# Kernel tuning notes

Hardware: AMD Instinct MI355X
Metric: run time of the kernel (lower is better)

The kernel has to match this reference:

```python
import jax, jax.numpy as jnp
import numpy as np

N = 50000
E = 800000
IN_C, HID_C, OUT_C = 128, 128, 64


def _glorot(key, shape, gain=1.0):
    fan_in, fan_out = shape[0], shape[1]
    lim = gain * np.sqrt(6.0 / (fan_in + fan_out))
    return jax.random.uniform(key, shape, jnp.float32, -lim, lim)


def setup_inputs() -> dict:
    key = jax.random.key(0)
    ks = jax.random.split(key, 16)
    relu_gain = float(np.sqrt(2.0))
    x = jax.random.normal(ks[0], (N, IN_C), jnp.float32)
    src = jax.random.randint(ks[1], (E,), 0, N, jnp.int64)
    dst = jax.random.randint(ks[2], (E,), 0, N, jnp.int64)
    # layer 0: NGNN_GCNConv(IN_C -> HID_C -> HID_C)
    W0 = _glorot(ks[3], (IN_C, HID_C))
    b0 = jnp.zeros((HID_C,), jnp.float32)
    fcW = _glorot(ks[4], (HID_C, HID_C), relu_gain)
    fcb = jax.random.uniform(ks[5], (HID_C,), jnp.float32, -1, 1) / np.sqrt(HID_C)
    fc2W = _glorot(ks[6], (HID_C, HID_C), relu_gain)
    fc2b = jax.random.uniform(ks[7], (HID_C,), jnp.float32, -1, 1) / np.sqrt(HID_C)
    # layer 1: GraphConv(HID_C -> HID_C)
    W1 = _glorot(ks[8], (HID_C, HID_C))
    b1 = jnp.zeros((HID_C,), jnp.float32)
    # layer 2: GraphConv(HID_C -> OUT_C)
    W2 = _glorot(ks[9], (HID_C, OUT_C))
    b2 = jnp.zeros((OUT_C,), jnp.float32)
    return dict(x=x, src=src, dst=dst, W0=W0, b0=b0, fcW=fcW, fcb=fcb,
                fc2W=fc2W, fc2b=fc2b, W1=W1, b1=b1, W2=W2, b2=b2)


def _degree_norms(src, dst):
    ones = jnp.ones((E,), jnp.float32)
    deg_out = jnp.clip(jax.ops.segment_sum(ones, src, num_segments=N), 1.0)
    deg_in = jnp.clip(jax.ops.segment_sum(ones, dst, num_segments=N), 1.0)
    return jax.lax.rsqrt(deg_out), jax.lax.rsqrt(deg_in)


def _graph_conv(x, W, b, src, dst, nsrc, ndst):
    # DGL GraphConv, norm='both': out = D_in^{-1/2} A (D_out^{-1/2} x W) + b
    h = (x * nsrc[:, None]) @ W            # [N, out_c]
    agg = jax.ops.segment_sum(h[src], dst, num_segments=N)  # gather + scatter-add
    return agg * ndst[:, None] + b


def reference(x, src, dst, W0, b0, fcW, fcb, fc2W, fc2b, W1, b1, W2, b2):
    nsrc, ndst = _degree_norms(src, dst)
    # layer 0: NGNN_GCNConv -> relu (dropout: eval-mode identity)
    h = _graph_conv(x, W0, b0, src, dst, nsrc, ndst)
    h = jax.nn.relu(h)
    h = jax.nn.relu(h @ fcW + fcb)
    h = h @ fc2W + fc2b
    h = jax.nn.relu(h)
    # layer 1: GraphConv -> relu
    h = jax.nn.relu(_graph_conv(h, W1, b1, src, dst, nsrc, ndst))
    # layer 2: GraphConv (no activation)
    return _graph_conv(h, W2, b2, src, dst, nsrc, ndst)
```

## Files before the change

kernel.cpp:

```cpp
#include <hip/hip_runtime.h>
#include <hip/hip_bf16.h>

#define NN 50000
#define NE 800000
#define PAD 56

typedef __attribute__((ext_vector_type(8))) short bf16x8;
typedef __attribute__((ext_vector_type(4))) float f32x4;
typedef __attribute__((ext_vector_type(8))) unsigned short u16x8;

__device__ __forceinline__ unsigned short f2bf(float f) {
    __hip_bfloat16 h = __float2bfloat16(f);
    return *(unsigned short*)&h;
}
__device__ __forceinline__ float bf2f(unsigned short u) {
    unsigned int w = ((unsigned int)u) << 16;
    return __uint_as_float(w);
}

__device__ __forceinline__ void split8(const float* __restrict__ p, bf16x8& h8, bf16x8& l8) {
    float4 v0 = *(const float4*)p;
    float4 v1 = *(const float4*)(p + 4);
    float f[8] = {v0.x, v0.y, v0.z, v0.w, v1.x, v1.y, v1.z, v1.w};
#pragma unroll
    for (int i = 0; i < 8; ++i) {
        unsigned short h = f2bf(f[i]);
        h8[i] = (short)h;
        l8[i] = (short)f2bf(f[i] - bf2f(h));
    }
}

#define SRC_BLK 64
#define SRC_CHUNK 12500
#define DST_BLK 160
#define DST_CHUNK 5000
#define DEG_WORDS 12500
#define GEMM0_BLK 782
#define CVW_ELEMS 57344
#define CVW_BLK 224

__global__ __launch_bounds__(256) void hists_kernel(
    const int* __restrict__ src, const int* __restrict__ dst,
    unsigned* __restrict__ psrc, unsigned* __restrict__ pdst,
    const float* __restrict__ x, const float* __restrict__ W0, unsigned short* __restrict__ Hb,
    const float* __restrict__ fcW, const float* __restrict__ fc2W,
    const float* __restrict__ W1, const float* __restrict__ W2,
    unsigned short* __restrict__ wp_hi, unsigned short* __restrict__ wp_lo) {
    __shared__ unsigned hist[DEG_WORDS];
    const int bid = blockIdx.x;
    const int tid = threadIdx.x;
    if (bid < SRC_BLK + DST_BLK) {
        const bool isSrc = bid < SRC_BLK;
        const int dblk = isSrc ? bid : bid - SRC_BLK;
        const int chunk = isSrc ? SRC_CHUNK : DST_CHUNK;
        const int* ep = isSrc ? (src + dblk * SRC_CHUNK) : (dst + dblk * DST_CHUNK);
        unsigned* outp = (isSrc ? psrc : pdst) + (size_t)dblk * DEG_WORDS;
        for (int i = tid; i < DEG_WORDS; i += 256) hist[i] = 0;
        __syncthreads();
        const int4* sp = (const int4*)ep;
        for (int i = tid; i < chunk / 4; i += 256) {
            int4 s = sp[i];
            atomicAdd(&hist[s.x >> 2], 1u << ((s.x & 3) * 8));
            atomicAdd(&hist[s.y >> 2], 1u << ((s.y & 3) * 8));
            atomicAdd(&hist[s.z >> 2], 1u << ((s.z & 3) * 8));
            atomicAdd(&hist[s.w >> 2], 1u << ((s.w & 3) * 8));
        }
        __syncthreads();
        for (int i = tid; i < DEG_WORDS; i += 256) outp[i] = hist[i];
    } else if (bid < SRC_BLK + DST_BLK + CVW_BLK) {
        int t = (bid - SRC_BLK - DST_BLK) * 256 + tid;
        if (t < CVW_ELEMS) {
            int mi = (t < 16384) ? 0 : (t < 32768) ? 1 : (t < 49152) ? 2 : 3;
            int beg = mi * 16384;
            int Cm = (mi == 3) ? 64 : 128;
            int loc = t - beg;
            int k = loc / Cm, c = loc % Cm;
            float v;
            switch (mi) {
                case 0: v = fcW[loc]; break;
                case 1: v = fc2W[loc]; break;
                case 2: v = W1[loc]; break;
                default: v = W2[loc]; break;
            }
            unsigned short h = f2bf(v);
            unsigned short l = f2bf(v - bf2f(h));
            int off = (((c >> 4) * 4 + (k >> 5)) * 64 + ((k & 31) >> 3) * 16 + (c & 15)) * 8 + (k & 7);
            wp_hi[beg + off] = h;
            wp_lo[beg + off] = l;
        }
    } else {
        const int gb = bid - SRC_BLK - DST_BLK - CVW_BLK;
        const int wave = tid >> 6;
        const int lane = tid & 63;
        const int m = lane & 15, kg = lane >> 4;
        const int r0 = gb * 64 + wave * 16;
        int ar = r0 + m;
        ar = (ar < NN) ? ar : (NN - 1);

        bf16x8 ah[4], al[4];
#pragma unroll
        for (int ks = 0; ks < 4; ++ks)
            split8(&x[(size_t)ar * 128 + ks * 32 + kg * 8], ah[ks], al[ks]);

#pragma unroll
        for (int ct = 0; ct < 8; ++ct) {
            f32x4 acc = {0.f, 0.f, 0.f, 0.f};
            const int n = ct * 16 + m;
#pragma unroll
            for (int ks = 0; ks < 4; ++ks) {
                float w[8];
#pragma unroll
                for (int i = 0; i < 8; ++i)
                    w[i] = W0[(size_t)(ks * 32 + kg * 8 + i) * 128 + n];
                bf16x8 bh, bl;
#pragma unroll
                for (int i = 0; i < 8; ++i) {
                    unsigned short h = f2bf(w[i]);
                    bh[i] = (short)h;
                    bl[i] = (short)f2bf(w[i] - bf2f(h));
                }
                acc = __builtin_amdgcn_mfma_f32_16x16x32_bf16(ah[ks], bh, acc, 0, 0, 0);
                acc = __builtin_amdgcn_mfma_f32_16x16x32_bf16(al[ks], bh, acc, 0, 0, 0);
                acc = __builtin_amdgcn_mfma_f32_16x16x32_bf16(ah[ks], bl, acc, 0, 0, 0);
            }
#pragma unroll
            for (int j = 0; j < 4; ++j) {
                const int ra = r0 + 4 * kg + j;
                if (ra < NN) Hb[(size_t)ra * 128 + n] = f2bf(acc[j]);
            }
        }
    }
}

__global__ __launch_bounds__(256) void merge_scan(unsigned* __restrict__ psrc,
                                                  unsigned* __restrict__ pdst,
                                                  int* __restrict__ degout,
                                                  int* __restrict__ cnt) {
    const int idx = blockIdx.x * 256 + threadIdx.x;
    if (idx >= DEG_WORDS) return;
    {
        int a0 = 0, a1 = 0, a2 = 0, a3 = 0;
#pragma unroll 8
        for (int p = 0; p < SRC_BLK; ++p) {
            unsigned w = psrc[(size_t)p * DEG_WORDS + idx];
            a0 += w & 0xFF; a1 += (w >> 8) & 0xFF; a2 += (w >> 16) & 0xFF; a3 += (w >> 24);
        }
        ((int4*)degout)[idx] = make_int4(a0, a1, a2, a3);
    }
    {
        int r0 = 0, r1 = 0, r2 = 0, r3 = 0;
#pragma unroll 8
        for (int p = 0; p < DST_BLK; ++p) {
            const size_t o = (size_t)p * DEG_WORDS + idx;
            unsigned w = pdst[o];
            pdst[o] = (unsigned)r0 | ((unsigned)r1 << 8) | ((unsigned)r2 << 16) | ((unsigned)r3 << 24);
            r0 += w & 0xFF; r1 += (w >> 8) & 0xFF; r2 += (w >> 16) & 0xFF; r3 += (w >> 24);
        }
        ((int4*)cnt)[idx] = make_int4(r0, r1, r2, r3);
    }
}

__global__ __launch_bounds__(256) void fillc_kernel(const int* __restrict__ src,
                                                    const int* __restrict__ dst,
                                                    const unsigned* __restrict__ pdst,
                                                    unsigned short* __restrict__ col) {
    __shared__ unsigned hist[DEG_WORDS];
    const int dblk = blockIdx.x;
    const int tid = threadIdx.x;
    const unsigned* bp = pdst + (size_t)dblk * DEG_WORDS;
    for (int i = tid; i < DEG_WORDS; i += 256) hist[i] = bp[i];
    __syncthreads();
    const int4* sp = (const int4*)(src + dblk * DST_CHUNK);
    const int4* dp = (const int4*)(dst + dblk * DST_CHUNK);
    for (int i = tid; i < DST_CHUNK / 4; i += 256) {
        int4 s = sp[i];
        int4 d = dp[i];
#pragma unroll
        for (int u = 0; u < 4; ++u) {
            const int dd = (u == 0) ? d.x : (u == 1) ? d.y : (u == 2) ? d.z : d.w;
            const int ss = (u == 0) ? s.x : (u == 1) ? s.y : (u == 2) ? s.z : s.w;
            const unsigned sh = (dd & 3) * 8;
            const unsigned old = atomicAdd(&hist[dd >> 2], 1u << sh);
            const int slot = (old >> sh) & 0xFF;
            col[dd * PAD + slot] = (unsigned short)ss;
        }
    }
}

__device__ __forceinline__ void t_write4(float (*T)[128], int lr, int c, float4 v) {
    *(float4*)&T[lr][(((c >> 2) ^ (lr & 31)) << 2)] = v;
}
__device__ __forceinline__ void t_write(float (*T)[128], int lr, int n, float v) {
    T[lr][((((n >> 2) ^ (lr & 31)) << 2) | (n & 3))] = v;
}
__device__ __forceinline__ void split8_lds(const float (*T)[128], int lr, int c, bf16x8& h8, bf16x8& l8) {
    const int c4 = c >> 2, xr = lr & 31;
    float4 v0 = *(const float4*)&T[lr][(c4 ^ xr) << 2];
    float4 v1 = *(const float4*)&T[lr][((c4 + 1) ^ xr) << 2];
    float f[8] = {v0.x, v0.y, v0.z, v0.w, v1.x, v1.y, v1.z, v1.w};
#pragma unroll
    for (int i = 0; i < 8; ++i) {
        unsigned short h = f2bf(f[i]);
        h8[i] = (short)h;
        l8[i] = (short)f2bf(f[i] - bf2f(h));
    }
}

template <int SCALE_SRC>
__device__ __forceinline__ void gather32_to_T(
    float (*T)[128], const unsigned short* __restrict__ H,
    const int* __restrict__ cnt, const int* __restrict__ degout,
    const unsigned short* __restrict__ colp, const float* __restrict__ bias,
    int r0, int N, int tid) {
    const int nl = tid >> 3;
    const int q  = tid & 7;
    int node = r0 + nl;
    node = (node < N) ? node : (N - 1);
    const int deg = cnt[node];
    const unsigned short* cl = colp + node * PAD;
    f32x4 acc[4];
#pragma unroll
    for (int v = 0; v < 4; ++v) acc[v] = (f32x4){0.f, 0.f, 0.f, 0.f};
    const int nch = (deg + 3) >> 2;
    for (int ch = 0; ch < nch; ++ch) {
        const int jb = ch * 4;
        ushort4 si = *(const ushort4*)&cl[jb];
        u16x8 h0[4], h1[4];
        float mm[4];
#pragma unroll
        for (int i = 0; i < 4; ++i) {
            const bool live = (jb + i < deg);
            const unsigned short sv = (i == 0) ? si.x : (i == 1) ? si.y : (i == 2) ? si.z : si.w;
            int s = live ? (int)sv : 0;
            const unsigned short* hp = &H[(size_t)s * 128 + q * 16];
            h0[i] = *(const u16x8*)hp;
            h1[i] = *(const u16x8*)(hp + 8);
            if (SCALE_SRC) {
                int dg = degout[s];
                float r = rsqrtf((float)(dg > 1 ? dg : 1));
                mm[i] = live ? r : 0.f;
            } else {
                mm[i] = live ? 1.f : 0.f;
            }
        }
#pragma unroll
        for (int i = 0; i < 4; ++i) {
#pragma unroll
            for (int k = 0; k < 8; ++k) {
                acc[k >> 2][k & 3] = fmaf(bf2f((unsigned short)h0[i][k]), mm[i], acc[k >> 2][k & 3]);
                acc[2 + (k >> 2)][k & 3] = fmaf(bf2f((unsigned short)h1[i][k]), mm[i], acc[2 + (k >> 2)][k & 3]);
            }
        }
    }
    const float scv = rsqrtf((float)(deg > 1 ? deg : 1));
#pragma unroll
    for (int v = 0; v < 4; ++v) {
        const int c = q * 16 + v * 4;
        const float4 b = *(const float4*)&bias[c];
        float4 o;
        o.x = fmaxf(acc[v][0] * scv + b.x, 0.f);
        o.y = fmaxf(acc[v][1] * scv + b.y, 0.f);
        o.z = fmaxf(acc[v][2] * scv + b.z, 0.f);
        o.w = fmaxf(acc[v][3] * scv + b.w, 0.f);
        t_write4(T, nl, c, o);
    }
}

#define TILE(WH, WL) \
    f32x4 acc = {0.f, 0.f, 0.f, 0.f}; \
    _Pragma("unroll") \
    for (int ks = 0; ks < 4; ++ks) { \
        const size_t base = ((size_t)(CT * 4 + ks) * 64 + lane) * 8; \
        bf16x8 bh = *(const bf16x8*)&WH[base]; \
        bf16x8 bl = *(const bf16x8*)&WL[base]; \
        acc = __builtin_amdgcn_mfma_f32_16x16x32_bf16(ah[ks], bh, acc, 0, 0, 0); \
        acc = __builtin_amdgcn_mfma_f32_16x16x32_bf16(al[ks], bh, acc, 0, 0, 0); \
        acc = __builtin_amdgcn_mfma_f32_16x16x32_bf16(ah[ks], bl, acc, 0, 0, 0); \
    }

#define LOAD_FRAGS_T() \
    _Pragma("unroll") \
    for (int ks = 0; ks < 4; ++ks) \
        split8_lds(T, wr + m, ks * 32 + kg * 8, ah[ks], al[ks]);

__global__ __launch_bounds__(256) void g0f3_kernel(
    const unsigned short* __restrict__ H,
    const int* __restrict__ cnt, const int* __restrict__ degout,
    const unsigned short* __restrict__ colp, const float* __restrict__ b0,
    const unsigned short* __restrict__ fwh, const unsigned short* __restrict__ fwl,
    const float* __restrict__ fcb,
    const unsigned short* __restrict__ f2h, const unsigned short* __restrict__ f2l,
    const float* __restrict__ fc2b,
    const unsigned short* __restrict__ w1h, const unsigned short* __restrict__ w1l,
    unsigned short* __restrict__ Yb, int N) {
    __shared__ float T[32][128];
    const int tid = threadIdx.x;
    const int wave = tid >> 6;
    const int lane = tid & 63;
    const int m = lane & 15, kg = lane >> 4;
    const int rowg = wave >> 1;
    const int colh = wave & 1;
    const int r0 = blockIdx.x * 32;
    const int wr = rowg * 16;

    gather32_to_T<1>(T, H, cnt, degout, colp, b0, r0, N, tid);
    __syncthreads();

    bf16x8 ah[4], al[4];
    LOAD_FRAGS_T();
    __syncthreads();

#pragma unroll
    for (int ct = 0; ct < 4; ++ct) {
        const int CT = colh * 4 + ct;
        TILE(fwh, fwl)
        const int n = CT * 16 + m;
        const float bb = fcb[n];
#pragma unroll
        for (int j = 0; j < 4; ++j)
            t_write(T, wr + 4 * kg + j, n, fmaxf(acc[j] + bb, 0.f));
    }
    __syncthreads();
    LOAD_FRAGS_T();
    __syncthreads();

#pragma unroll
    for (int ct = 0; ct < 4; ++ct) {
        const int CT = colh * 4 + ct;
        TILE(f2h, f2l)
        const int n = CT * 16 + m;
        const float bb = fc2b[n];
#pragma unroll
        for (int j = 0; j < 4; ++j)
            t_write(T, wr + 4 * kg + j, n, fmaxf(acc[j] + bb, 0.f));
    }
    __syncthreads();
    LOAD_FRAGS_T();

#pragma unroll
    for (int ct = 0; ct < 4; ++ct) {
        const int CT = colh * 4 + ct;
        TILE(w1h, w1l)
        const int n = CT * 16 + m;
#pragma unroll
        for (int j = 0; j < 4; ++j) {
            const int ra = r0 + wr + 4 * kg + j;
            if (ra < N) {
                int dg = degout[ra];
                Yb[(size_t)ra * 128 + n] = f2bf(acc[j] * rsqrtf((float)(dg > 1 ? dg : 1)));
            }
        }
    }
}

__global__ __launch_bounds__(256) void g1g2_kernel(
    const unsigned short* __restrict__ H,
    const int* __restrict__ cnt, const int* __restrict__ degout,
    const unsigned short* __restrict__ colp, const float* __restrict__ b1,
    const unsigned short* __restrict__ w2h, const unsigned short* __restrict__ w2l,
    unsigned short* __restrict__ Yb, int N) {
    __shared__ float T[32][128];
    const int tid = threadIdx.x;
    const int wave = tid >> 6;
    const int lane = tid & 63;
    const int m = lane & 15, kg = lane >> 4;
    const int rowg = wave >> 1;
    const int colh = wave & 1;
    const int r0 = blockIdx.x * 32;
    const int wr = rowg * 16;

    gather32_to_T<0>(T, H, cnt, degout, colp, b1, r0, N, tid);
    __syncthreads();

    bf16x8 ah[4], al[4];
    LOAD_FRAGS_T();

#pragma unroll
    for (int ct = 0; ct < 2; ++ct) {
        const int CT = colh * 2 + ct;
        TILE(w2h, w2l)
        const int n = CT * 16 + m;
#pragma unroll
        for (int j = 0; j < 4; ++j) {
            const int ra = r0 + wr + 4 * kg + j;
            if (ra < N) {
                int dg = degout[ra];
                Yb[(size_t)ra * 64 + n] = f2bf(acc[j] * rsqrtf((float)(dg > 1 ? dg : 1)));
            }
        }
    }
}

__global__ __launch_bounds__(256) void gather2_kernel(
    const unsigned short* __restrict__ H, const int* __restrict__ cnt,
    const unsigned short* __restrict__ col,
    const float* __restrict__ bias, float* __restrict__ OUT, int N) {
    constexpr int C = 64, LPN = 8, NPB = 32;
    const int node = blockIdx.x * NPB + threadIdx.x / LPN;
    const int q = threadIdx.x % LPN;
    if (node >= N) return;
    const int deg = cnt[node];
    const unsigned short* cl = col + node * PAD;
    float acc[8];
#pragma unroll
    for (int k = 0; k < 8; ++k) acc[k] = 0.f;
    const int nch = (deg + 7) >> 3;
    for (int ch = 0; ch < nch; ++ch) {
        const int jb = ch * 8;
        u16x8 si = *(const u16x8*)&cl[jb];
        u16x8 hv[8];
        float mm[8];
#pragma unroll
        for (int i = 0; i < 8; ++i) {
            const bool live = (jb + i < deg);
            int s = live ? (int)si[i] : 0;
            hv[i] = *(const u16x8*)&H[(size_t)s * C + q * 8];
            mm[i] = live ? 1.f : 0.f;
        }
#pragma unroll
        for (int i = 0; i < 8; ++i) {
#pragma unroll
            for (int k = 0; k < 8; ++k)
                acc[k] = fmaf(bf2f((unsigned short)hv[i][k]), mm[i], acc[k]);
        }
    }
    const float scv = rsqrtf((float)(deg > 1 ? deg : 1));
    const int cb = q * 8;
    float4 o0, o1;
    const float4 b0 = *(const float4*)&bias[cb];
    const float4 b1 = *(const float4*)&bias[cb + 4];
    o0.x = acc[0] * scv + b0.x; o0.y = acc[1] * scv + b0.y;
    o0.z = acc[2] * scv + b0.z; o0.w = acc[3] * scv + b0.w;
    o1.x = acc[4] * scv + b1.x; o1.y = acc[5] * scv + b1.y;
    o1.z = acc[6] * scv + b1.z; o1.w = acc[7] * scv + b1.w;
    *(float4*)&OUT[(size_t)node * C + cb] = o0;
    *(float4*)&OUT[(size_t)node * C + cb + 4] = o1;
}

extern "C" void kernel_launch(void* const* d_in, const int* in_sizes, int n_in,
                              void* d_out, int out_size, void* d_ws, size_t ws_size,
                              hipStream_t stream) {
    const float* x    = (const float*)d_in[0];
    const int*   src  = (const int*)d_in[1];
    const int*   dst  = (const int*)d_in[2];
    const float* W0   = (const float*)d_in[3];
    const float* b0   = (const float*)d_in[4];
    const float* fcW  = (const float*)d_in[5];
    const float* fcb  = (const float*)d_in[6];
    const float* fc2W = (const float*)d_in[7];
    const float* fc2b = (const float*)d_in[8];
    const float* W1   = (const float*)d_in[9];
    const float* b1   = (const float*)d_in[10];
    const float* W2   = (const float*)d_in[11];
    const float* b2   = (const float*)d_in[12];
    float* out = (float*)d_out;

    char* ws = (char*)d_ws;
    int* cnt    = (int*)ws;
    int* degout = cnt + NN;
    unsigned short* col = (unsigned short*)(degout + NN);
    unsigned short* wp_hi = col + (size_t)NN * PAD;
    unsigned short* wp_lo = wp_hi + CVW_ELEMS;
    size_t p = ((size_t)(2 * NN) * 4 + (size_t)NN * PAD * 2 + (size_t)CVW_ELEMS * 4 + 255) & ~(size_t)255;
    unsigned* psrc = (unsigned*)(ws + p);
    unsigned* pdst = psrc + (size_t)SRC_BLK * DEG_WORDS;
    size_t p1 = (p + (size_t)(SRC_BLK + DST_BLK) * DEG_WORDS * 4 + 255) & ~(size_t)255;
    unsigned short* Hb  = (unsigned short*)(ws + p1);
    unsigned short* Hb2 = Hb + (size_t)NN * 128;

    const unsigned short *fwh = wp_hi,          *fwl = wp_lo;
    const unsigned short *f2h = wp_hi + 16384,  *f2l = wp_lo + 16384;
    const unsigned short *w1h = wp_hi + 32768,  *w1l = wp_lo + 32768;
    const unsigned short *w2h = wp_hi + 49152,  *w2l = wp_lo + 49152;

    hists_kernel<<<SRC_BLK + DST_BLK + CVW_BLK + GEMM0_BLK, 256, 0, stream>>>(
        src, dst, psrc, pdst, x, W0, Hb, fcW, fc2W, W1, W2, wp_hi, wp_lo);
    merge_scan<<<(DEG_WORDS + 255) / 256, 256, 0, stream>>>(psrc, pdst, degout, cnt);
    fillc_kernel<<<DST_BLK, 256, 0, stream>>>(src, dst, pdst, col);

    const int g32 = (NN + 31) / 32;

    g0f3_kernel<<<g32, 256, 0, stream>>>(Hb, cnt, degout, col, b0,
                                         fwh, fwl, fcb, f2h, f2l, fc2b, w1h, w1l, Hb2, NN);
    g1g2_kernel<<<g32, 256, 0, stream>>>(Hb2, cnt, degout, col, b1, w2h, w2l, Hb, NN);
    gather2_kernel<<<g32, 256, 0, stream>>>(Hb, cnt, col, b2, out, NN);
}
```

Measured before the change: 161.2 us.

## Halve rows per block in fused gather+MLP kernels, 16 lanes per node

```diff
diff --git a/kernel.cpp b/kernel.cpp
--- a/kernel.cpp
+++ b/kernel.cpp
@@ -207,34 +207,30 @@
 }
 
 template <int SCALE_SRC>
-__device__ __forceinline__ void gather32_to_T(
+__device__ __forceinline__ void gather16_to_T(
     float (*T)[128], const unsigned short* __restrict__ H,
     const int* __restrict__ cnt, const int* __restrict__ degout,
     const unsigned short* __restrict__ colp, const float* __restrict__ bias,
     int r0, int N, int tid) {
-    const int nl = tid >> 3;
-    const int q  = tid & 7;
+    const int nl = tid >> 4;
+    const int q  = tid & 15;
     int node = r0 + nl;
     node = (node < N) ? node : (N - 1);
     const int deg = cnt[node];
     const unsigned short* cl = colp + node * PAD;
-    f32x4 acc[4];
-#pragma unroll
-    for (int v = 0; v < 4; ++v) acc[v] = (f32x4){0.f, 0.f, 0.f, 0.f};
-    const int nch = (deg + 3) >> 2;
+    f32x4 acc0 = {0.f, 0.f, 0.f, 0.f};
+    f32x4 acc1 = {0.f, 0.f, 0.f, 0.f};
+    const int nch = (deg + 7) >> 3;
     for (int ch = 0; ch < nch; ++ch) {
-        const int jb = ch * 4;
-        ushort4 si = *(const ushort4*)&cl[jb];
-        u16x8 h0[4], h1[4];
-        float mm[4];
-#pragma unroll
-        for (int i = 0; i < 4; ++i) {
+        const int jb = ch * 8;
+        u16x8 si = *(const u16x8*)&cl[jb];
+        u16x8 hv[8];
+        float mm[8];
+#pragma unroll
+        for (int i = 0; i < 8; ++i) {
             const bool live = (jb + i < deg);
-            const unsigned short sv = (i == 0) ? si.x : (i == 1) ? si.y : (i == 2) ? si.z : si.w;
-            int s = live ? (int)sv : 0;
-            const unsigned short* hp = &H[(size_t)s * 128 + q * 16];
-            h0[i] = *(const u16x8*)hp;
-            h1[i] = *(const u16x8*)(hp + 8);
+            int s = live ? (int)si[i] : 0;
+            hv[i] = *(const u16x8*)&H[(size_t)s * 128 + q * 8];
             if (SCALE_SRC) {
                 int dg = degout[s];
                 float r = rsqrtf((float)(dg > 1 ? dg : 1));
@@ -244,26 +240,29 @@
             }
         }
 #pragma unroll
-        for (int i = 0; i < 4; ++i) {
-#pragma unroll
-            for (int k = 0; k < 8; ++k) {
-                acc[k >> 2][k & 3] = fmaf(bf2f((unsigned short)h0[i][k]), mm[i], acc[k >> 2][k & 3]);
-                acc[2 + (k >> 2)][k & 3] = fmaf(bf2f((unsigned short)h1[i][k]), mm[i], acc[2 + (k >> 2)][k & 3]);
+        for (int i = 0; i < 8; ++i) {
+#pragma unroll
+            for (int k = 0; k < 4; ++k) {
+                acc0[k] = fmaf(bf2f((unsigned short)hv[i][k]), mm[i], acc0[k]);
+                acc1[k] = fmaf(bf2f((unsigned short)hv[i][4 + k]), mm[i], acc1[k]);
             }
         }
     }
     const float scv = rsqrtf((float)(deg > 1 ? deg : 1));
-#pragma unroll
-    for (int v = 0; v < 4; ++v) {
-        const int c = q * 16 + v * 4;
-        const float4 b = *(const float4*)&bias[c];
-        float4 o;
-        o.x = fmaxf(acc[v][0] * scv + b.x, 0.f);
-        o.y = fmaxf(acc[v][1] * scv + b.y, 0.f);
-        o.z = fmaxf(acc[v][2] * scv + b.z, 0.f);
-        o.w = fmaxf(acc[v][3] * scv + b.w, 0.f);
-        t_write4(T, nl, c, o);
-    }
+    const int c = q * 8;
+    const float4 b0 = *(const float4*)&bias[c];
+    const float4 b1 = *(const float4*)&bias[c + 4];
+    float4 o0, o1;
+    o0.x = fmaxf(acc0[0] * scv + b0.x, 0.f);
+    o0.y = fmaxf(acc0[1] * scv + b0.y, 0.f);
+    o0.z = fmaxf(acc0[2] * scv + b0.z, 0.f);
+    o0.w = fmaxf(acc0[3] * scv + b0.w, 0.f);
+    o1.x = fmaxf(acc1[0] * scv + b1.x, 0.f);
+    o1.y = fmaxf(acc1[1] * scv + b1.y, 0.f);
+    o1.z = fmaxf(acc1[2] * scv + b1.z, 0.f);
+    o1.w = fmaxf(acc1[3] * scv + b1.w, 0.f);
+    t_write4(T, nl, c, o0);
+    t_write4(T, nl, c + 4, o1);
 }
 
 #define TILE(WH, WL) \
@@ -281,7 +280,7 @@
 #define LOAD_FRAGS_T() \
     _Pragma("unroll") \
     for (int ks = 0; ks < 4; ++ks) \
-        split8_lds(T, wr + m, ks * 32 + kg * 8, ah[ks], al[ks]);
+        split8_lds(T, m, ks * 32 + kg * 8, ah[ks], al[ks]);
 
 __global__ __launch_bounds__(256) void g0f3_kernel(
     const unsigned short* __restrict__ H,
@@ -293,17 +292,14 @@
     const float* __restrict__ fc2b,
     const unsigned short* __restrict__ w1h, const unsigned short* __restrict__ w1l,
     unsigned short* __restrict__ Yb, int N) {
-    __shared__ float T[32][128];
+    __shared__ float T[16][128];
     const int tid = threadIdx.x;
     const int wave = tid >> 6;
     const int lane = tid & 63;
     const int m = lane & 15, kg = lane >> 4;
-    const int rowg = wave >> 1;
-    const int colh = wave & 1;
-    const int r0 = blockIdx.x * 32;
-    const int wr = rowg * 16;
-
-    gather32_to_T<1>(T, H, cnt, degout, colp, b0, r0, N, tid);
+    const int r0 = blockIdx.x * 16;
+
+    gather16_to_T<1>(T, H, cnt, degout, colp, b0, r0, N, tid);
     __syncthreads();
 
     bf16x8 ah[4], al[4];
@@ -311,40 +307,40 @@
     __syncthreads();
 
 #pragma unroll
-    for (int ct = 0; ct < 4; ++ct) {
-        const int CT = colh * 4 + ct;
+    for (int ct = 0; ct < 2; ++ct) {
+        const int CT = wave * 2 + ct;
         TILE(fwh, fwl)
         const int n = CT * 16 + m;
         const float bb = fcb[n];
 #pragma unroll
         for (int j = 0; j < 4; ++j)
-            t_write(T, wr + 4 * kg + j, n, fmaxf(acc[j] + bb, 0.f));
+            t_write(T, 4 * kg + j, n, fmaxf(acc[j] + bb, 0.f));
     }
     __syncthreads();
     LOAD_FRAGS_T();
     __syncthreads();
 
 #pragma unroll
-    for (int ct = 0; ct < 4; ++ct) {
-        const int CT = colh * 4 + ct;
+    for (int ct = 0; ct < 2; ++ct) {
+        const int CT = wave * 2 + ct;
         TILE(f2h, f2l)
         const int n = CT * 16 + m;
         const float bb = fc2b[n];
 #pragma unroll
         for (int j = 0; j < 4; ++j)
-            t_write(T, wr + 4 * kg + j, n, fmaxf(acc[j] + bb, 0.f));
+            t_write(T, 4 * kg + j, n, fmaxf(acc[j] + bb, 0.f));
     }
     __syncthreads();
     LOAD_FRAGS_T();
 
 #pragma unroll
-    for (int ct = 0; ct < 4; ++ct) {
-        const int CT = colh * 4 + ct;
+    for (int ct = 0; ct < 2; ++ct) {
+        const int CT = wave * 2 + ct;
         TILE(w1h, w1l)
         const int n = CT * 16 + m;
 #pragma unroll
         for (int j = 0; j < 4; ++j) {
-            const int ra = r0 + wr + 4 * kg + j;
+            const int ra = r0 + 4 * kg + j;
             if (ra < N) {
                 int dg = degout[ra];
                 Yb[(size_t)ra * 128 + n] = f2bf(acc[j] * rsqrtf((float)(dg > 1 ? dg : 1)));
@@ -359,30 +355,26 @@
     const unsigned short* __restrict__ colp, const float* __restrict__ b1,
     const unsigned short* __restrict__ w2h, const unsigned short* __restrict__ w2l,
     unsigned short* __restrict__ Yb, int N) {
-    __shared__ float T[32][128];
+    __shared__ float T[16][128];
     const int tid = threadIdx.x;
     const int wave = tid >> 6;
     const int lane = tid & 63;
     const int m = lane & 15, kg = lane >> 4;
-    const int rowg = wave >> 1;
-    const int colh = wave & 1;
-    const int r0 = blockIdx.x * 32;
-    const int wr = rowg * 16;
-
-    gather32_to_T<0>(T, H, cnt, degout, colp, b1, r0, N, tid);
+    const int r0 = blockIdx.x * 16;
+
+    gather16_to_T<0>(T, H, cnt, degout, colp, b1, r0, N, tid);
     __syncthreads();
 
     bf16x8 ah[4], al[4];
     LOAD_FRAGS_T();
 
-#pragma unroll
-    for (int ct = 0; ct < 2; ++ct) {
-        const int CT = colh * 2 + ct;
+    {
+        const int CT = wave;
         TILE(w2h, w2l)
         const int n = CT * 16 + m;
 #pragma unroll
         for (int j = 0; j < 4; ++j) {
-            const int ra = r0 + wr + 4 * kg + j;
+            const int ra = r0 + 4 * kg + j;
             if (ra < N) {
                 int dg = degout[ra];
                 Yb[(size_t)ra * 64 + n] = f2bf(acc[j] * rsqrtf((float)(dg > 1 ? dg : 1)));
@@ -478,10 +470,11 @@
     merge_scan<<<(DEG_WORDS + 255) / 256, 256, 0, stream>>>(psrc, pdst, degout, cnt);
     fillc_kernel<<<DST_BLK, 256, 0, stream>>>(src, dst, pdst, col);
 
+    const int g16 = (NN + 15) / 16;
     const int g32 = (NN + 31) / 32;
 
-    g0f3_kernel<<<g32, 256, 0, stream>>>(Hb, cnt, degout, col, b0,
+    g0f3_kernel<<<g16, 256, 0, stream>>>(Hb, cnt, degout, col, b0,
                                          fwh, fwl, fcb, f2h, f2l, fc2b, w1h, w1l, Hb2, NN);
-    g1g2_kernel<<<g32, 256, 0, stream>>>(Hb2, cnt, degout, col, b1, w2h, w2l, Hb, NN);
+    g1g2_kernel<<<g16, 256, 0, stream>>>(Hb2, cnt, degout, col, b1, w2h, w2l, Hb, NN);
     gather2_kernel<<<g32, 256, 0, stream>>>(Hb, cnt, col, b2, out, NN);
 }
```

Measured after the change: 152.5 us. 1.06x faster.

## Give each wave both row tiles in dense layers and even out src histogram split

Applied to the files above, without the earlier changes.

```diff
diff --git a/kernel.cpp b/kernel.cpp
--- a/kernel.cpp
+++ b/kernel.cpp
@@ -30,10 +30,8 @@
     }
 }
 
-#define SRC_BLK 64
-#define SRC_CHUNK 12500
-#define DST_BLK 160
-#define DST_CHUNK 5000
+#define HIST_BLK 160
+#define HIST_CHUNK 5000
 #define DEG_WORDS 12500
 #define GEMM0_BLK 782
 #define CVW_ELEMS 57344
@@ -49,16 +47,15 @@
     __shared__ unsigned hist[DEG_WORDS];
     const int bid = blockIdx.x;
     const int tid = threadIdx.x;
-    if (bid < SRC_BLK + DST_BLK) {
-        const bool isSrc = bid < SRC_BLK;
-        const int dblk = isSrc ? bid : bid - SRC_BLK;
-        const int chunk = isSrc ? SRC_CHUNK : DST_CHUNK;
-        const int* ep = isSrc ? (src + dblk * SRC_CHUNK) : (dst + dblk * DST_CHUNK);
+    if (bid < 2 * HIST_BLK) {
+        const bool isSrc = bid < HIST_BLK;
+        const int dblk = isSrc ? bid : bid - HIST_BLK;
+        const int* ep = (isSrc ? src : dst) + dblk * HIST_CHUNK;
         unsigned* outp = (isSrc ? psrc : pdst) + (size_t)dblk * DEG_WORDS;
         for (int i = tid; i < DEG_WORDS; i += 256) hist[i] = 0;
         __syncthreads();
         const int4* sp = (const int4*)ep;
-        for (int i = tid; i < chunk / 4; i += 256) {
+        for (int i = tid; i < HIST_CHUNK / 4; i += 256) {
             int4 s = sp[i];
             atomicAdd(&hist[s.x >> 2], 1u << ((s.x & 3) * 8));
             atomicAdd(&hist[s.y >> 2], 1u << ((s.y & 3) * 8));
@@ -67,8 +64,8 @@
         }
         __syncthreads();
         for (int i = tid; i < DEG_WORDS; i += 256) outp[i] = hist[i];
-    } else if (bid < SRC_BLK + DST_BLK + CVW_BLK) {
-        int t = (bid - SRC_BLK - DST_BLK) * 256 + tid;
+    } else if (bid < 2 * HIST_BLK + CVW_BLK) {
+        int t = (bid - 2 * HIST_BLK) * 256 + tid;
         if (t < CVW_ELEMS) {
             int mi = (t < 16384) ? 0 : (t < 32768) ? 1 : (t < 49152) ? 2 : 3;
             int beg = mi * 16384;
@@ -89,7 +86,7 @@
             wp_lo[beg + off] = l;
         }
     } else {
-        const int gb = bid - SRC_BLK - DST_BLK - CVW_BLK;
+        const int gb = bid - 2 * HIST_BLK - CVW_BLK;
         const int wave = tid >> 6;
         const int lane = tid & 63;
         const int m = lane & 15, kg = lane >> 4;
@@ -141,7 +138,7 @@
     {
         int a0 = 0, a1 = 0, a2 = 0, a3 = 0;
 #pragma unroll 8
-        for (int p = 0; p < SRC_BLK; ++p) {
+        for (int p = 0; p < HIST_BLK; ++p) {
             unsigned w = psrc[(size_t)p * DEG_WORDS + idx];
             a0 += w & 0xFF; a1 += (w >> 8) & 0xFF; a2 += (w >> 16) & 0xFF; a3 += (w >> 24);
         }
@@ -150,7 +147,7 @@
     {
         int r0 = 0, r1 = 0, r2 = 0, r3 = 0;
 #pragma unroll 8
-        for (int p = 0; p < DST_BLK; ++p) {
+        for (int p = 0; p < HIST_BLK; ++p) {
             const size_t o = (size_t)p * DEG_WORDS + idx;
             unsigned w = pdst[o];
             pdst[o] = (unsigned)r0 | ((unsigned)r1 << 8) | ((unsigned)r2 << 16) | ((unsigned)r3 << 24);
@@ -170,9 +167,9 @@
     const unsigned* bp = pdst + (size_t)dblk * DEG_WORDS;
     for (int i = tid; i < DEG_WORDS; i += 256) hist[i] = bp[i];
     __syncthreads();
-    const int4* sp = (const int4*)(src + dblk * DST_CHUNK);
-    const int4* dp = (const int4*)(dst + dblk * DST_CHUNK);
-    for (int i = tid; i < DST_CHUNK / 4; i += 256) {
+    const int4* sp = (const int4*)(src + dblk * HIST_CHUNK);
+    const int4* dp = (const int4*)(dst + dblk * HIST_CHUNK);
+    for (int i = tid; i < HIST_CHUNK / 4; i += 256) {
         int4 s = sp[i];
         int4 d = dp[i];
 #pragma unroll
@@ -266,22 +263,28 @@
     }
 }
 
-#define TILE(WH, WL) \
-    f32x4 acc = {0.f, 0.f, 0.f, 0.f}; \
+#define TILE2(WH, WL) \
+    f32x4 acc0 = {0.f, 0.f, 0.f, 0.f}; \
+    f32x4 acc1 = {0.f, 0.f, 0.f, 0.f}; \
     _Pragma("unroll") \
     for (int ks = 0; ks < 4; ++ks) { \
         const size_t base = ((size_t)(CT * 4 + ks) * 64 + lane) * 8; \
         bf16x8 bh = *(const bf16x8*)&WH[base]; \
         bf16x8 bl = *(const bf16x8*)&WL[base]; \
-        acc = __builtin_amdgcn_mfma_f32_16x16x32_bf16(ah[ks], bh, acc, 0, 0, 0); \
-        acc = __builtin_amdgcn_mfma_f32_16x16x32_bf16(al[ks], bh, acc, 0, 0, 0); \
-        acc = __builtin_amdgcn_mfma_f32_16x16x32_bf16(ah[ks], bl, acc, 0, 0, 0); \
-    }
-
-#define LOAD_FRAGS_T() \
+        acc0 = __builtin_amdgcn_mfma_f32_16x16x32_bf16(ah0[ks], bh, acc0, 0, 0, 0); \
+        acc1 = __builtin_amdgcn_mfma_f32_16x16x32_bf16(ah1[ks], bh, acc1, 0, 0, 0); \
+        acc0 = __builtin_amdgcn_mfma_f32_16x16x32_bf16(al0[ks], bh, acc0, 0, 0, 0); \
+        acc1 = __builtin_amdgcn_mfma_f32_16x16x32_bf16(al1[ks], bh, acc1, 0, 0, 0); \
+        acc0 = __builtin_amdgcn_mfma_f32_16x16x32_bf16(ah0[ks], bl, acc0, 0, 0, 0); \
+        acc1 = __builtin_amdgcn_mfma_f32_16x16x32_bf16(ah1[ks], bl, acc1, 0, 0, 0); \
+    }
+
+#define LOAD_FRAGS2() \
     _Pragma("unroll") \
-    for (int ks = 0; ks < 4; ++ks) \
-        split8_lds(T, wr + m, ks * 32 + kg * 8, ah[ks], al[ks]);
+    for (int ks = 0; ks < 4; ++ks) { \
+        split8_lds(T, m,      ks * 32 + kg * 8, ah0[ks], al0[ks]); \
+        split8_lds(T, 16 + m, ks * 32 + kg * 8, ah1[ks], al1[ks]); \
+    }
 
 __global__ __launch_bounds__(256) void g0f3_kernel(
     const unsigned short* __restrict__ H,
@@ -298,56 +301,62 @@
     const int wave = tid >> 6;
     const int lane = tid & 63;
     const int m = lane & 15, kg = lane >> 4;
-    const int rowg = wave >> 1;
-    const int colh = wave & 1;
     const int r0 = blockIdx.x * 32;
-    const int wr = rowg * 16;
 
     gather32_to_T<1>(T, H, cnt, degout, colp, b0, r0, N, tid);
     __syncthreads();
 
-    bf16x8 ah[4], al[4];
-    LOAD_FRAGS_T();
-    __syncthreads();
-
-#pragma unroll
-    for (int ct = 0; ct < 4; ++ct) {
-        const int CT = colh * 4 + ct;
-        TILE(fwh, fwl)
+    bf16x8 ah0[4], al0[4], ah1[4], al1[4];
+    LOAD_FRAGS2();
+    __syncthreads();
+
+#pragma unroll
+    for (int ct = 0; ct < 2; ++ct) {
+        const int CT = wave * 2 + ct;
+        TILE2(fwh, fwl)
         const int n = CT * 16 + m;
         const float bb = fcb[n];
 #pragma unroll
-        for (int j = 0; j < 4; ++j)
-            t_write(T, wr + 4 * kg + j, n, fmaxf(acc[j] + bb, 0.f));
-    }
-    __syncthreads();
-    LOAD_FRAGS_T();
-    __syncthreads();
-
-#pragma unroll
-    for (int ct = 0; ct < 4; ++ct) {
-        const int CT = colh * 4 + ct;
-        TILE(f2h, f2l)
+        for (int j = 0; j < 4; ++j) {
+            t_write(T, 4 * kg + j,      n, fmaxf(acc0[j] + bb, 0.f));
+            t_write(T, 16 + 4 * kg + j, n, fmaxf(acc1[j] + bb, 0.f));
+        }
+    }
+    __syncthreads();
+    LOAD_FRAGS2();
+    __syncthreads();
+
+#pragma unroll
+    for (int ct = 0; ct < 2; ++ct) {
+        const int CT = wave * 2 + ct;
+        TILE2(f2h, f2l)
         const int n = CT * 16 + m;
         const float bb = fc2b[n];
 #pragma unroll
-        for (int j = 0; j < 4; ++j)
-            t_write(T, wr + 4 * kg + j, n, fmaxf(acc[j] + bb, 0.f));
-    }
-    __syncthreads();
-    LOAD_FRAGS_T();
-
-#pragma unroll
-    for (int ct = 0; ct < 4; ++ct) {
-        const int CT = colh * 4 + ct;
-        TILE(w1h, w1l)
+        for (int j = 0; j < 4; ++j) {
+            t_write(T, 4 * kg + j,      n, fmaxf(acc0[j] + bb, 0.f));
+            t_write(T, 16 + 4 * kg + j, n, fmaxf(acc1[j] + bb, 0.f));
+        }
+    }
+    __syncthreads();
+    LOAD_FRAGS2();
+
+#pragma unroll
+    for (int ct = 0; ct < 2; ++ct) {
+        const int CT = wave * 2 + ct;
+        TILE2(w1h, w1l)
         const int n = CT * 16 + m;
 #pragma unroll
         for (int j = 0; j < 4; ++j) {
-            const int ra = r0 + wr + 4 * kg + j;
+            const int ra = r0 + 4 * kg + j;
             if (ra < N) {
                 int dg = degout[ra];
-                Yb[(size_t)ra * 128 + n] = f2bf(acc[j] * rsqrtf((float)(dg > 1 ? dg : 1)));
+                Yb[(size_t)ra * 128 + n] = f2bf(acc0[j] * rsqrtf((float)(dg > 1 ? dg : 1)));
+            }
+            const int rb = r0 + 16 + 4 * kg + j;
+            if (rb < N) {
+                int dg = degout[rb];
+                Yb[(size_t)rb * 128 + n] = f2bf(acc1[j] * rsqrtf((float)(dg > 1 ? dg : 1)));
             }
         }
     }
@@ -364,28 +373,29 @@
     const int wave = tid >> 6;
     const int lane = tid & 63;
     const int m = lane & 15, kg = lane >> 4;
-    const int rowg = wave >> 1;
-    const int colh = wave & 1;
     const int r0 = blockIdx.x * 32;
-    const int wr = rowg * 16;
 
     gather32_to_T<0>(T, H, cnt, degout, colp, b1, r0, N, tid);
     __syncthreads();
 
-    bf16x8 ah[4], al[4];
-    LOAD_FRAGS_T();
-
-#pragma unroll
-    for (int ct = 0; ct < 2; ++ct) {
-        const int CT = colh * 2 + ct;
-        TILE(w2h, w2l)
+    bf16x8 ah0[4], al0[4], ah1[4], al1[4];
+    LOAD_FRAGS2();
+
+    {
+        const int CT = wave;
+        TILE2(w2h, w2l)
         const int n = CT * 16 + m;
 #pragma unroll
         for (int j = 0; j < 4; ++j) {
-            const int ra = r0 + wr + 4 * kg + j;
+            const int ra = r0 + 4 * kg + j;
             if (ra < N) {
                 int dg = degout[ra];
-                Yb[(size_t)ra * 64 + n] = f2bf(acc[j] * rsqrtf((float)(dg > 1 ? dg : 1)));
+                Yb[(size_t)ra * 64 + n] = f2bf(acc0[j] * rsqrtf((float)(dg > 1 ? dg : 1)));
+            }
+            const int rb = r0 + 16 + 4 * kg + j;
+            if (rb < N) {
+                int dg = degout[rb];
+                Yb[(size_t)rb * 64 + n] = f2bf(acc1[j] * rsqrtf((float)(dg > 1 ? dg : 1)));
             }
         }
     }
@@ -463,8 +473,8 @@
     unsigned short* wp_lo = wp_hi + CVW_ELEMS;
     size_t p = ((size_t)(2 * NN) * 4 + (size_t)NN * PAD * 2 + (size_t)CVW_ELEMS * 4 + 255) & ~(size_t)255;
     unsigned* psrc = (unsigned*)(ws + p);
-    unsigned* pdst = psrc + (size_t)SRC_BLK * DEG_WORDS;
-    size_t p1 = (p + (size_t)(SRC_BLK + DST_BLK) * DEG_WORDS * 4 + 255) & ~(size_t)255;
+    unsigned* pdst = psrc + (size_t)HIST_BLK * DEG_WORDS;
+    size_t p1 = (p + (size_t)2 * HIST_BLK * DEG_WORDS * 4 + 255) & ~(size_t)255;
     unsigned short* Hb  = (unsigned short*)(ws + p1);
     unsigned short* Hb2 = Hb + (size_t)NN * 128;
 
@@ -473,10 +483,10 @@
     const unsigned short *w1h = wp_hi + 32768,  *w1l = wp_lo + 32768;
     const unsigned short *w2h = wp_hi + 49152,  *w2l = wp_lo + 49152;
 
-    hists_kernel<<<SRC_BLK + DST_BLK + CVW_BLK + GEMM0_BLK, 256, 0, stream>>>(
+    hists_kernel<<<2 * HIST_BLK + CVW_BLK + GEMM0_BLK, 256, 0, stream>>>(
         src, dst, psrc, pdst, x, W0, Hb, fcW, fc2W, W1, W2, wp_hi, wp_lo);
     merge_scan<<<(DEG_WORDS + 255) / 256, 256, 0, stream>>>(psrc, pdst, degout, cnt);
-    fillc_kernel<<<DST_BLK, 256, 0, stream>>>(src, dst, pdst, col);
+    fillc_kernel<<<HIST_BLK, 256, 0, stream>>>(src, dst, pdst, col);
 
     const int g32 = (NN + 31) / 32;
 
```

New measurement: 162.8 us. About the same (+1.0%).
